# Kernel tuning notes

Hardware: AMD Instinct MI355X
Metric: run time of the kernel (lower is better)

## Reference

```python
import jax, jax.numpy as jnp
import numpy as np

IMG = 224
NUM_VIEWS = 6
K = 5  # splat kernel size (5x5 = 25 offsets)


def setup_inputs() -> dict:
    key = jax.random.key(0)
    points = jax.random.normal(key, (16, 32768, 3), dtype=jnp.float32)
    return {"points": points}


def _render(points):
    B, N, _ = points.shape
    deg2rad = jnp.pi / 180.0
    az = jnp.linspace(0.0, 360.0, NUM_VIEWS + 1)[:-1] * deg2rad          # (V,)
    el = jnp.array([0.0, 30.0, -30.0, 0.0, 0.0, 0.0])[:NUM_VIEWS] * deg2rad

    # 5x5 splat offsets in normalized coords, matching torch meshgrid(ij) + stack([dx,dy])
    off = jnp.linspace(-2.0 / IMG, 2.0 / IMG, K)
    dyg, dxg = jnp.meshgrid(off, off, indexing="ij")
    koff = jnp.stack([dxg, dyg], axis=-1).reshape(-1, 2)                  # (25, 2)

    def one_view(a, e):
        x, y, z = points[..., 0], points[..., 1], points[..., 2]
        x_rot = x * jnp.cos(a) - z * jnp.sin(a)
        z_rot = x * jnp.sin(a) + z * jnp.cos(a)
        y_rot = y * jnp.cos(e) - z_rot * jnp.sin(e)
        z_fin = y * jnp.sin(e) + z_rot * jnp.cos(e)                       # (B, N)
        p2d = jnp.stack([x_rot, y_rot], axis=-1)                          # (B, N, 2)

        zmin = jnp.min(z_fin, axis=1, keepdims=True)
        zmax = jnp.max(z_fin, axis=1, keepdims=True)
        feat = 0.3 + 0.7 * (z_fin - zmin) / (zmax - zmin + 1e-6)          # (B, N), in [0.3, 1.0]

        coords = p2d[:, :, None, :] + koff[None, None, :, :]              # (B, N, 25, 2)
        # torch .long() truncates toward zero; astype(int32) does too
        px = ((coords[..., 0] + 1.0) * 0.5 * (IMG - 1)).astype(jnp.int32)
        py = ((coords[..., 1] + 1.0) * 0.5 * (IMG - 1)).astype(jnp.int32)
        valid = (px >= 0) & (px < IMG) & (py >= 0) & (py < IMG)
        # invalid splats routed out-of-bounds and dropped by the scatter
        idx = jnp.where(valid, py * IMG + px, IMG * IMG).reshape(B, -1)   # (B, N*25)
        f = jnp.broadcast_to(feat[:, :, None], (B, N, K * K)).reshape(B, -1)

        def splat(i, fv):
            return jnp.zeros(IMG * IMG, dtype=points.dtype).at[i].max(fv, mode="drop")

        img = jax.vmap(splat)(idx, f).reshape(B, IMG, IMG)
        # all 3 channels receive the identical feature values
        return jnp.broadcast_to(img[:, None], (B, 3, IMG, IMG))

    views = jax.vmap(one_view)(az, el)                                    # (V, B, 3, H, W)
    return jnp.transpose(views, (1, 0, 2, 3, 4))                          # (B, V, 3, H, W)


def reference(points) -> jnp.ndarray:
    return _render(points)
```

## Files before the change

kernel.cpp:

```cpp
#include <hip/hip_runtime.h>
#include <math.h>

#define IMG    224
#define NVIEWS 6
#define BATCH  16
#define NPTS   32768
#define PLANE  (IMG * IMG)
#define HROWS  112
#define TILE_ELEMS (HROWS * IMG)
#define NTHREADS 1024
#define NWG (BATCH * NVIEWS * 2)

typedef float fx4 __attribute__((ext_vector_type(4)));

struct ViewTrig {
    float sa[NVIEWS], ca[NVIEWS], se[NVIEWS], ce[NVIEWS];
    float off0, off4;
};

__device__ __forceinline__ float fmul_(float a, float b) {
#pragma clang fp contract(off)
    return a * b;
}
__device__ __forceinline__ float fadd_(float a, float b) {
#pragma clang fp contract(off)
    return a + b;
}
__device__ __forceinline__ float fsub_(float a, float b) {
#pragma clang fp contract(off)
    return a - b;
}
__device__ __forceinline__ int pix_(float c) {
    return (int)fmul_(fmul_(fadd_(c, 1.0f), 0.5f), 223.0f);
}

__device__ __forceinline__ unsigned fmap_(float f) {
    unsigned b = __float_as_uint(f);
    return b ^ ((unsigned)((int)b >> 31) | 0x80000000u);
}
__device__ __forceinline__ float fmap_inv_(unsigned u) {
    unsigned b = (u & 0x80000000u) ? (u ^ 0x80000000u) : ~u;
    return __uint_as_float(b);
}

__global__ __launch_bounds__(NTHREADS, 4) void render_kernel(
    const float* __restrict__ pts, float* __restrict__ out, ViewTrig vt)
{
    extern __shared__ __align__(16) unsigned tile[];
    __shared__ float smin[NTHREADS / 64], smax[NTHREADS / 64];

    const int bid  = blockIdx.x;
    const int xcd  = bid & 7;
    const int slot = bid >> 3;
    const int hi   = (slot >= 12) ? 1 : 0;
    const int b    = xcd + 8 * hi;
    const int vh   = slot - 12 * hi;
    const int v    = vh >> 1;
    const int h    = vh & 1;
    const int bv   = b * NVIEWS + v;
    const int row0 = h * HROWS;

    const float sa = vt.sa[v], ca = vt.ca[v], se = vt.se[v], ce = vt.ce[v];
    const float off0 = vt.off0, off4 = vt.off4;
    const float4* p4 = (const float4*)(pts + (size_t)b * NPTS * 3);

    {
        int4* t4 = (int4*)tile;
        for (int i = threadIdx.x; i < TILE_ELEMS / 4; i += NTHREADS)
            t4[i] = make_int4(0, 0, 0, 0);
    }
    __syncthreads();

    float zmin = INFINITY, zmax = -INFINITY;

    auto do_point = [&](float x, float y, float z) {
        const float zr = fadd_(fmul_(x, sa), fmul_(z, ca));
        const float yr = fsub_(fmul_(y, ce), fmul_(zr, se));
        const float xr = fsub_(fmul_(x, ca), fmul_(z, sa));

        const int y0i = max(pix_(fadd_(yr, off0)), row0);
        const int y1i = min(pix_(fadd_(yr, off4)), row0 + HROWS - 1);
        const int x0i = max(pix_(fadd_(xr, off0)), 0);
        const int x1i = min(pix_(fadd_(xr, off4)), IMG - 1);

        const float zf = fmaf(zr, ce, y * se);
        zmin = fminf(zmin, zf);
        zmax = fmaxf(zmax, zf);
        const unsigned fz = fmap_(zf);

        #pragma unroll
        for (int dy = 0; dy < 3; ++dy) {
            const int ry = y0i + dy;
            const bool yok = (ry <= y1i);
            const int base = (ry - row0) * IMG;
            #pragma unroll
            for (int dx = 0; dx < 3; ++dx) {
                const int cx = x0i + dx;
                if (yok && (cx <= x1i)) atomicMax(&tile[base + cx], fz);
            }
        }
    };

    #pragma unroll
    for (int k = 0; k < NPTS / (4 * NTHREADS); ++k) {
        const int g = threadIdx.x + k * NTHREADS;
        const float4 A = p4[3 * g + 0];
        const float4 B = p4[3 * g + 1];
        const float4 C = p4[3 * g + 2];
        do_point(A.x, A.y, A.z);
        do_point(A.w, B.x, B.y);
        do_point(B.z, B.w, C.x);
        do_point(C.y, C.z, C.w);
    }

    for (int o = 32; o > 0; o >>= 1) {
        zmin = fminf(zmin, __shfl_down(zmin, o, 64));
        zmax = fmaxf(zmax, __shfl_down(zmax, o, 64));
    }
    const int wave = threadIdx.x >> 6;
    if ((threadIdx.x & 63) == 0) { smin[wave] = zmin; smax[wave] = zmax; }
    __syncthreads();
    if (threadIdx.x == 0) {
        float mn = smin[0], mx = smax[0];
        for (int w = 1; w < NTHREADS / 64; ++w) {
            mn = fminf(mn, smin[w]);
            mx = fmaxf(mx, smax[w]);
        }
        smin[0] = mn; smax[0] = mx;
    }
    __syncthreads();
    const float scale = 0.7f / ((smax[0] - smin[0]) + 1e-6f);
    const float bias  = 0.3f - smin[0] * scale;

    float* dst = out + ((size_t)bv * 3) * PLANE + (size_t)row0 * IMG;
    const uint4* src = (const uint4*)tile;
    for (int i = threadIdx.x; i < TILE_ELEMS / 4; i += NTHREADS) {
        const uint4 u = src[i];
        fx4 f;
        f.x = (u.x == 0u) ? 0.0f : fmaf(fmap_inv_(u.x), scale, bias);
        f.y = (u.y == 0u) ? 0.0f : fmaf(fmap_inv_(u.y), scale, bias);
        f.z = (u.z == 0u) ? 0.0f : fmaf(fmap_inv_(u.z), scale, bias);
        f.w = (u.w == 0u) ? 0.0f : fmaf(fmap_inv_(u.w), scale, bias);
        #pragma unroll
        for (int c = 0; c < 3; ++c)
            __builtin_nontemporal_store(f, (fx4*)(dst + (size_t)c * PLANE) + i);
    }
}

extern "C" void kernel_launch(void* const* d_in, const int* in_sizes, int n_in,
                              void* d_out, int out_size, void* d_ws, size_t ws_size,
                              hipStream_t stream)
{
    const float* pts = (const float*)d_in[0];
    float* out = (float*)d_out;

    ViewTrig vt;
    const float d2r = (float)(M_PI / 180.0);
    const float el_deg[NVIEWS] = {0.0f, 30.0f, -30.0f, 0.0f, 0.0f, 0.0f};
    for (int v = 0; v < NVIEWS; ++v) {
        float a = (float)(60 * v) * d2r;
        float e = el_deg[v] * d2r;
        vt.sa[v] = (float)sin((double)a);
        vt.ca[v] = (float)cos((double)a);
        vt.se[v] = (float)sin((double)e);
        vt.ce[v] = (float)cos((double)e);
    }
    {
        const float s = (float)(2.0 / 224.0);
        vt.off0 = -s;
        vt.off4 = s;
    }

    (void)hipFuncSetAttribute(reinterpret_cast<const void*>(render_kernel),
                              hipFuncAttributeMaxDynamicSharedMemorySize,
                              TILE_ELEMS * (int)sizeof(int));

    render_kernel<<<NWG, NTHREADS, TILE_ELEMS * sizeof(int), stream>>>(pts, out, vt);
}
```

Measured before the change: 91.54 us.

## Split rendering into binning prep pass and per-half-tile splat pass

Adds a prep kernel that projects each point once per view, computes its clamped pixel footprint, and appends a compact (depth, packed-bbox) record to a per-half-image list using wave-aggregated atomics. It also writes partial z min/max values. The render kernel then reads only the records that touch its half and skips the rotation math. This removes the duplicated projection work and the processing of points that fall outside each half-image tile. In exchange it adds a memset, a second launch, and global memory traffic for the lists and counters.

```diff
diff --git a/kernel.cpp b/kernel.cpp
--- a/kernel.cpp
+++ b/kernel.cpp
@@ -8,8 +8,10 @@
 #define PLANE  (IMG * IMG)
 #define HROWS  112
 #define TILE_ELEMS (HROWS * IMG)
-#define NTHREADS 1024
-#define NWG (BATCH * NVIEWS * 2)
+#define NT     1024
+#define NWG    (BATCH * NVIEWS * 2)
+#define CAP    32768
+#define NLISTS (BATCH * NVIEWS * 2)
 
 typedef float fx4 __attribute__((ext_vector_type(4)));
 
@@ -43,11 +45,112 @@
     return __uint_as_float(b);
 }
 
-__global__ __launch_bounds__(NTHREADS, 4) void render_kernel(
-    const float* __restrict__ pts, float* __restrict__ out, ViewTrig vt)
+__device__ __forceinline__ int lane_prefix_(unsigned long long m) {
+    return __builtin_amdgcn_mbcnt_hi((unsigned)(m >> 32),
+           __builtin_amdgcn_mbcnt_lo((unsigned)m, 0));
+}
+
+__global__ __launch_bounds__(NT, 4) void prep_kernel(
+    const float* __restrict__ pts, unsigned* __restrict__ counters,
+    uint2* __restrict__ lists, float* __restrict__ mm, ViewTrig vt)
+{
+    __shared__ float smin[NT / 64], smax[NT / 64];
+
+    const int bid  = blockIdx.x;
+    const int xcd  = bid & 7;
+    const int slot = bid >> 3;
+    const int hi   = (slot >= 12) ? 1 : 0;
+    const int b    = xcd + 8 * hi;
+    const int vc   = slot - 12 * hi;
+    const int v    = vc >> 1;
+    const int c    = vc & 1;
+    const int bv   = b * NVIEWS + v;
+
+    const float sa = vt.sa[v], ca = vt.ca[v], se = vt.se[v], ce = vt.ce[v];
+    const float off0 = vt.off0, off4 = vt.off4;
+    const float4* p4 = (const float4*)(pts + ((size_t)b * NPTS + (size_t)c * (NPTS / 2)) * 3);
+
+    const int lane = threadIdx.x & 63;
+    float zmin = INFINITY, zmax = -INFINITY;
+
+    auto do_point = [&](float x, float y, float z) {
+        const float zr = fadd_(fmul_(x, sa), fmul_(z, ca));
+        const float yr = fsub_(fmul_(y, ce), fmul_(zr, se));
+        const float xr = fsub_(fmul_(x, ca), fmul_(z, sa));
+
+        const int x0i = pix_(fadd_(xr, off0));
+        const int x1i = pix_(fadd_(xr, off4));
+        const int y0i = pix_(fadd_(yr, off0));
+        const int y1i = pix_(fadd_(yr, off4));
+
+        const float zf = fmaf(zr, ce, y * se);
+        zmin = fminf(zmin, zf);
+        zmax = fmaxf(zmax, zf);
+        const unsigned fz = fmap_(zf);
+
+        const int cx0 = min(max(x0i, 0), IMG - 1);
+        const int cx1 = min(max(x1i, 0), IMG - 1);
+        const int cy0 = min(max(y0i, 0), IMG - 1);
+        const int cy1 = min(max(y1i, 0), IMG - 1);
+        const unsigned pk = (unsigned)cx0 | ((unsigned)cx1 << 8) |
+                            ((unsigned)cy0 << 16) | ((unsigned)cy1 << 24);
+
+        const bool xok = (x1i >= 0) && (x0i <= IMG - 1);
+        const bool h0 = xok && (y0i <= HROWS - 1) && (y1i >= 0);
+        const bool h1 = xok && (y1i >= HROWS) && (y0i <= IMG - 1);
+
+        #pragma unroll
+        for (int h = 0; h < 2; ++h) {
+            const bool pred = h ? h1 : h0;
+            const unsigned long long m = __ballot(pred);
+            if (m == 0ull) continue;
+            const int cnt = __popcll(m);
+            const int leader = __builtin_ctzll(m);
+            unsigned tmp = 0;
+            if (lane == leader)
+                tmp = atomicAdd(&counters[bv * 2 + h], (unsigned)cnt);
+            const unsigned base = __shfl(tmp, leader, 64);
+            if (pred)
+                lists[(size_t)(bv * 2 + h) * CAP + base + lane_prefix_(m)]
+                    = make_uint2(fz, pk);
+        }
+    };
+
+    #pragma unroll
+    for (int k = 0; k < (NPTS / 2) / (4 * NT); ++k) {
+        const int g = threadIdx.x + k * NT;
+        const float4 A = p4[3 * g + 0];
+        const float4 B = p4[3 * g + 1];
+        const float4 C = p4[3 * g + 2];
+        do_point(A.x, A.y, A.z);
+        do_point(A.w, B.x, B.y);
+        do_point(B.z, B.w, C.x);
+        do_point(C.y, C.z, C.w);
+    }
+
+    for (int o = 32; o > 0; o >>= 1) {
+        zmin = fminf(zmin, __shfl_down(zmin, o, 64));
+        zmax = fmaxf(zmax, __shfl_down(zmax, o, 64));
+    }
+    const int wave = threadIdx.x >> 6;
+    if (lane == 0) { smin[wave] = zmin; smax[wave] = zmax; }
+    __syncthreads();
+    if (threadIdx.x == 0) {
+        float mn = smin[0], mx = smax[0];
+        for (int w = 1; w < NT / 64; ++w) {
+            mn = fminf(mn, smin[w]);
+            mx = fmaxf(mx, smax[w]);
+        }
+        mm[(bv * 2 + c) * 2 + 0] = mn;
+        mm[(bv * 2 + c) * 2 + 1] = mx;
+    }
+}
+
+__global__ __launch_bounds__(NT, 4) void render_kernel(
+    const unsigned* __restrict__ counters, const uint2* __restrict__ lists,
+    const float* __restrict__ mm, float* __restrict__ out)
 {
     extern __shared__ __align__(16) unsigned tile[];
-    __shared__ float smin[NTHREADS / 64], smax[NTHREADS / 64];
 
     const int bid  = blockIdx.x;
     const int xcd  = bid & 7;
@@ -60,81 +163,50 @@
     const int bv   = b * NVIEWS + v;
     const int row0 = h * HROWS;
 
-    const float sa = vt.sa[v], ca = vt.ca[v], se = vt.se[v], ce = vt.ce[v];
-    const float off0 = vt.off0, off4 = vt.off4;
-    const float4* p4 = (const float4*)(pts + (size_t)b * NPTS * 3);
-
     {
         int4* t4 = (int4*)tile;
-        for (int i = threadIdx.x; i < TILE_ELEMS / 4; i += NTHREADS)
+        for (int i = threadIdx.x; i < TILE_ELEMS / 4; i += NT)
             t4[i] = make_int4(0, 0, 0, 0);
     }
     __syncthreads();
 
-    float zmin = INFINITY, zmax = -INFINITY;
-
-    auto do_point = [&](float x, float y, float z) {
-        const float zr = fadd_(fmul_(x, sa), fmul_(z, ca));
-        const float yr = fsub_(fmul_(y, ce), fmul_(zr, se));
-        const float xr = fsub_(fmul_(x, ca), fmul_(z, sa));
-
-        const int y0i = max(pix_(fadd_(yr, off0)), row0);
-        const int y1i = min(pix_(fadd_(yr, off4)), row0 + HROWS - 1);
-        const int x0i = max(pix_(fadd_(xr, off0)), 0);
-        const int x1i = min(pix_(fadd_(xr, off4)), IMG - 1);
-
-        const float zf = fmaf(zr, ce, y * se);
-        zmin = fminf(zmin, zf);
-        zmax = fmaxf(zmax, zf);
-        const unsigned fz = fmap_(zf);
+    const int li = bv * 2 + h;
+    const unsigned cnt = counters[li];
+    const uint2* lp = lists + (size_t)li * CAP;
+
+    for (unsigned i = threadIdx.x; i < cnt; i += NT) {
+        const uint2 e = lp[i];
+        const unsigned fz = e.x;
+        const unsigned pk = e.y;
+        const int cx0 = pk & 255;
+        const int cx1 = (pk >> 8) & 255;
+        const int cy0 = (pk >> 16) & 255;
+        const int cy1 = pk >> 24;
+        const int r0 = max(cy0, row0);
+        const int r1 = min(cy1, row0 + HROWS - 1);
 
         #pragma unroll
         for (int dy = 0; dy < 3; ++dy) {
-            const int ry = y0i + dy;
-            const bool yok = (ry <= y1i);
+            const int ry = r0 + dy;
+            const bool yok = (ry <= r1);
             const int base = (ry - row0) * IMG;
             #pragma unroll
             for (int dx = 0; dx < 3; ++dx) {
-                const int cx = x0i + dx;
-                if (yok && (cx <= x1i)) atomicMax(&tile[base + cx], fz);
+                const int cx = cx0 + dx;
+                if (yok && (cx <= cx1)) atomicMax(&tile[base + cx], fz);
             }
         }
-    };
-
-    #pragma unroll
-    for (int k = 0; k < NPTS / (4 * NTHREADS); ++k) {
-        const int g = threadIdx.x + k * NTHREADS;
-        const float4 A = p4[3 * g + 0];
-        const float4 B = p4[3 * g + 1];
-        const float4 C = p4[3 * g + 2];
-        do_point(A.x, A.y, A.z);
-        do_point(A.w, B.x, B.y);
-        do_point(B.z, B.w, C.x);
-        do_point(C.y, C.z, C.w);
-    }
-
-    for (int o = 32; o > 0; o >>= 1) {
-        zmin = fminf(zmin, __shfl_down(zmin, o, 64));
-        zmax = fmaxf(zmax, __shfl_down(zmax, o, 64));
-    }
-    const int wave = threadIdx.x >> 6;
-    if ((threadIdx.x & 63) == 0) { smin[wave] = zmin; smax[wave] = zmax; }
+    }
     __syncthreads();
-    if (threadIdx.x == 0) {
-        float mn = smin[0], mx = smax[0];
-        for (int w = 1; w < NTHREADS / 64; ++w) {
-            mn = fminf(mn, smin[w]);
-            mx = fmaxf(mx, smax[w]);
-        }
-        smin[0] = mn; smax[0] = mx;
-    }
-    __syncthreads();
-    const float scale = 0.7f / ((smax[0] - smin[0]) + 1e-6f);
-    const float bias  = 0.3f - smin[0] * scale;
+
+    const float zmn = fminf(mm[(bv * 2 + 0) * 2 + 0], mm[(bv * 2 + 1) * 2 + 0]);
+    const float zmx = fmaxf(mm[(bv * 2 + 0) * 2 + 1], mm[(bv * 2 + 1) * 2 + 1]);
+    const float scale = 0.7f / ((zmx - zmn) + 1e-6f);
+    const float bias  = 0.3f - zmn * scale;
 
     float* dst = out + ((size_t)bv * 3) * PLANE + (size_t)row0 * IMG;
     const uint4* src = (const uint4*)tile;
-    for (int i = threadIdx.x; i < TILE_ELEMS / 4; i += NTHREADS) {
+    for (int i = threadIdx.x; i < TILE_ELEMS / 4; i += NT) {
         const uint4 u = src[i];
         fx4 f;
         f.x = (u.x == 0u) ? 0.0f : fmaf(fmap_inv_(u.x), scale, bias);
@@ -153,6 +225,10 @@
 {
     const float* pts = (const float*)d_in[0];
     float* out = (float*)d_out;
+
+    unsigned* counters = (unsigned*)d_ws;
+    uint2*    lists    = (uint2*)((char*)d_ws + 1024);
+    float*    mm       = (float*)((char*)d_ws + 1024 + (size_t)NLISTS * CAP * 8);
 
     ViewTrig vt;
     const float d2r = (float)(M_PI / 180.0);
@@ -175,5 +251,8 @@
                               hipFuncAttributeMaxDynamicSharedMemorySize,
                               TILE_ELEMS * (int)sizeof(int));
 
-    render_kernel<<<NWG, NTHREADS, TILE_ELEMS * sizeof(int), stream>>>(pts, out, vt);
-}
+    hipMemsetAsync(counters, 0, NLISTS * sizeof(unsigned), stream);
+
+    prep_kernel<<<NWG, NT, 0, stream>>>(pts, counters, lists, mm, vt);
+    render_kernel<<<NWG, NT, TILE_ELEMS * sizeof(int), stream>>>(counters, lists, mm, out);
+}
```

Measured after the change: 250.8 us. 2.74x slower.

## Compact in-tile points per wave via LDS queue before splatting atomics

Applied to the files above, without the earlier changes.

Each block renders half an image, so about half the points fall outside its rows, yet those lanes still occupy wave slots during the atomic loop. The kernel now uses a ballot and mbcnt prefix to push only in-range points into a per-wave LDS queue, and drains 64 queued splats at once so every lane does useful atomicMax work. This is meant to cut divergence and wasted atomic issue slots. In exchange it adds LDS writes and reads, ballot and popcount work per point, and some extra LDS footprint.

```diff
diff --git a/kernel.cpp b/kernel.cpp
--- a/kernel.cpp
+++ b/kernel.cpp
@@ -8,8 +8,10 @@
 #define PLANE  (IMG * IMG)
 #define HROWS  112
 #define TILE_ELEMS (HROWS * IMG)
-#define NTHREADS 1024
-#define NWG (BATCH * NVIEWS * 2)
+#define NT     1024
+#define NWAVES (NT / 64)
+#define QCAP   128
+#define NWG    (BATCH * NVIEWS * 2)
 
 typedef float fx4 __attribute__((ext_vector_type(4)));
 
@@ -43,11 +45,17 @@
     return __uint_as_float(b);
 }
 
-__global__ __launch_bounds__(NTHREADS, 4) void render_kernel(
+__device__ __forceinline__ int lane_prefix_(unsigned long long m) {
+    return __builtin_amdgcn_mbcnt_hi((unsigned)(m >> 32),
+           __builtin_amdgcn_mbcnt_lo((unsigned)m, 0));
+}
+
+__global__ __launch_bounds__(NT, 4) void render_kernel(
     const float* __restrict__ pts, float* __restrict__ out, ViewTrig vt)
 {
     extern __shared__ __align__(16) unsigned tile[];
-    __shared__ float smin[NTHREADS / 64], smax[NTHREADS / 64];
+    __shared__ uint2 wq[NWAVES][QCAP];
+    __shared__ float smin[NWAVES], smax[NWAVES];
 
     const int bid  = blockIdx.x;
     const int xcd  = bid & 7;
@@ -59,51 +67,78 @@
     const int h    = vh & 1;
     const int bv   = b * NVIEWS + v;
     const int row0 = h * HROWS;
+    const int row1 = row0 + HROWS - 1;
 
     const float sa = vt.sa[v], ca = vt.ca[v], se = vt.se[v], ce = vt.ce[v];
     const float off0 = vt.off0, off4 = vt.off4;
     const float4* p4 = (const float4*)(pts + (size_t)b * NPTS * 3);
 
+    const int lane = threadIdx.x & 63;
+    const int wave = threadIdx.x >> 6;
+
     {
         int4* t4 = (int4*)tile;
-        for (int i = threadIdx.x; i < TILE_ELEMS / 4; i += NTHREADS)
+        for (int i = threadIdx.x; i < TILE_ELEMS / 4; i += NT)
             t4[i] = make_int4(0, 0, 0, 0);
     }
     __syncthreads();
 
     float zmin = INFINITY, zmax = -INFINITY;
+    unsigned qcnt = 0;
+
+    auto drain64 = [&]() {
+        qcnt -= 64;
+        const uint2 e = wq[wave][qcnt + lane];
+        const unsigned fz = e.x, pk = e.y;
+        const int cx0 = pk & 255;
+        const int cx1 = (pk >> 8) & 255;
+        const int r0 = max((int)((pk >> 16) & 255), row0) - row0;
+        const int r1 = min((int)(pk >> 24), row1) - row0;
+        #pragma unroll
+        for (int dy = 0; dy < 3; ++dy) {
+            const int ry = r0 + dy;
+            const bool yok = (ry <= r1);
+            #pragma unroll
+            for (int dx = 0; dx < 3; ++dx) {
+                const int cx = cx0 + dx;
+                if (yok && (cx <= cx1)) atomicMax(&tile[ry * IMG + cx], fz);
+            }
+        }
+    };
 
     auto do_point = [&](float x, float y, float z) {
         const float zr = fadd_(fmul_(x, sa), fmul_(z, ca));
         const float yr = fsub_(fmul_(y, ce), fmul_(zr, se));
         const float xr = fsub_(fmul_(x, ca), fmul_(z, sa));
 
-        const int y0i = max(pix_(fadd_(yr, off0)), row0);
-        const int y1i = min(pix_(fadd_(yr, off4)), row0 + HROWS - 1);
-        const int x0i = max(pix_(fadd_(xr, off0)), 0);
-        const int x1i = min(pix_(fadd_(xr, off4)), IMG - 1);
+        const int x0i = pix_(fadd_(xr, off0));
+        const int x1i = pix_(fadd_(xr, off4));
+        const int y0i = pix_(fadd_(yr, off0));
+        const int y1i = pix_(fadd_(yr, off4));
 
         const float zf = fmaf(zr, ce, y * se);
         zmin = fminf(zmin, zf);
         zmax = fmaxf(zmax, zf);
-        const unsigned fz = fmap_(zf);
-
-        #pragma unroll
-        for (int dy = 0; dy < 3; ++dy) {
-            const int ry = y0i + dy;
-            const bool yok = (ry <= y1i);
-            const int base = (ry - row0) * IMG;
-            #pragma unroll
-            for (int dx = 0; dx < 3; ++dx) {
-                const int cx = x0i + dx;
-                if (yok && (cx <= x1i)) atomicMax(&tile[base + cx], fz);
-            }
-        }
+
+        const bool pred = (x1i >= 0) && (x0i <= IMG - 1) &&
+                          (y1i >= row0) && (y0i <= row1);
+        const unsigned long long m = __ballot(pred);
+        if (pred) {
+            const int cx0 = min(max(x0i, 0), IMG - 1);
+            const int cx1 = min(max(x1i, 0), IMG - 1);
+            const int cy0 = min(max(y0i, 0), IMG - 1);
+            const int cy1 = min(max(y1i, 0), IMG - 1);
+            const unsigned pk = (unsigned)cx0 | ((unsigned)cx1 << 8) |
+                                ((unsigned)cy0 << 16) | ((unsigned)cy1 << 24);
+            wq[wave][qcnt + lane_prefix_(m)] = make_uint2(fmap_(zf), pk);
+        }
+        qcnt += (unsigned)__popcll(m);
+        if (qcnt >= 64) drain64();
     };
 
     #pragma unroll
-    for (int k = 0; k < NPTS / (4 * NTHREADS); ++k) {
-        const int g = threadIdx.x + k * NTHREADS;
+    for (int k = 0; k < NPTS / (4 * NT); ++k) {
+        const int g = threadIdx.x + k * NT;
         const float4 A = p4[3 * g + 0];
         const float4 B = p4[3 * g + 1];
         const float4 C = p4[3 * g + 2];
@@ -113,16 +148,34 @@
         do_point(C.y, C.z, C.w);
     }
 
+    if (lane < (int)qcnt) {
+        const uint2 e = wq[wave][lane];
+        const unsigned fz = e.x, pk = e.y;
+        const int cx0 = pk & 255;
+        const int cx1 = (pk >> 8) & 255;
+        const int r0 = max((int)((pk >> 16) & 255), row0) - row0;
+        const int r1 = min((int)(pk >> 24), row1) - row0;
+        #pragma unroll
+        for (int dy = 0; dy < 3; ++dy) {
+            const int ry = r0 + dy;
+            const bool yok = (ry <= r1);
+            #pragma unroll
+            for (int dx = 0; dx < 3; ++dx) {
+                const int cx = cx0 + dx;
+                if (yok && (cx <= cx1)) atomicMax(&tile[ry * IMG + cx], fz);
+            }
+        }
+    }
+
     for (int o = 32; o > 0; o >>= 1) {
         zmin = fminf(zmin, __shfl_down(zmin, o, 64));
         zmax = fmaxf(zmax, __shfl_down(zmax, o, 64));
     }
-    const int wave = threadIdx.x >> 6;
-    if ((threadIdx.x & 63) == 0) { smin[wave] = zmin; smax[wave] = zmax; }
+    if (lane == 0) { smin[wave] = zmin; smax[wave] = zmax; }
     __syncthreads();
     if (threadIdx.x == 0) {
         float mn = smin[0], mx = smax[0];
-        for (int w = 1; w < NTHREADS / 64; ++w) {
+        for (int w = 1; w < NWAVES; ++w) {
             mn = fminf(mn, smin[w]);
             mx = fmaxf(mx, smax[w]);
         }
@@ -134,7 +187,7 @@
 
     float* dst = out + ((size_t)bv * 3) * PLANE + (size_t)row0 * IMG;
     const uint4* src = (const uint4*)tile;
-    for (int i = threadIdx.x; i < TILE_ELEMS / 4; i += NTHREADS) {
+    for (int i = threadIdx.x; i < TILE_ELEMS / 4; i += NT) {
         const uint4 u = src[i];
         fx4 f;
         f.x = (u.x == 0u) ? 0.0f : fmaf(fmap_inv_(u.x), scale, bias);
@@ -175,5 +228,5 @@
                               hipFuncAttributeMaxDynamicSharedMemorySize,
                               TILE_ELEMS * (int)sizeof(int));
 
-    render_kernel<<<NWG, NTHREADS, TILE_ELEMS * sizeof(int), stream>>>(pts, out, vt);
-}
+    render_kernel<<<NWG, NT, TILE_ELEMS * sizeof(int), stream>>>(pts, out, vt);
+}
```

Result: faster. 88.41 us, median of 2 (-3.4%).
